# Kernel optimization log

Hardware: AMD Instinct MI355X
Metric: run time of the kernel (lower is better)

The kernel has to match this reference:

```python
import jax, jax.numpy as jnp
import numpy as np

B, S, D_MODEL, NUM_HEADS, MAX_LEN = 4, 1024, 1024, 16, 1024
D_HEAD = D_MODEL // NUM_HEADS


def _skew(QEr):
    # QEr: (b, h, s, s). Music-Transformer skew: pad one col on the left,
    # reshape swapping the last two dims, drop the first row.
    b, h, r, c = QEr.shape
    padded = jnp.pad(QEr, ((0, 0), (0, 0), (0, 0), (1, 0)))  # (b,h,r,c+1)
    reshaped = padded.reshape(b, h, c + 1, r)
    return reshaped[:, :, 1:, :]  # (b,h,s,s)


def setup_inputs() -> dict:
    key = jax.random.key(0)
    ks = jax.random.split(key, 8)
    sc = 1.0 / np.sqrt(D_MODEL).astype(np.float32)
    return {
        "x": jax.random.normal(ks[0], (B, S, D_MODEL), jnp.float32),
        "Wq": jax.random.normal(ks[1], (D_MODEL, D_MODEL), jnp.float32) * sc,
        "bq": jnp.zeros((D_MODEL,), jnp.float32),
        "Wk": jax.random.normal(ks[2], (D_MODEL, D_MODEL), jnp.float32) * sc,
        "bk": jnp.zeros((D_MODEL,), jnp.float32),
        "Wv": jax.random.normal(ks[3], (D_MODEL, D_MODEL), jnp.float32) * sc,
        "bv": jnp.zeros((D_MODEL,), jnp.float32),
        "Er": jax.random.normal(ks[4], (MAX_LEN, D_HEAD), jnp.float32),
    }


def reference(x, Wq, bq, Wk, bk, Wv, bv, Er):
    b, s, _ = x.shape
    h, dh = NUM_HEADS, D_HEAD
    # projections -> (b, h, s, dh). Weights stored [in, out] (equiv. to torch W.T).
    q = (x @ Wq + bq).reshape(b, s, h, dh).transpose(0, 2, 1, 3)
    k = (x @ Wk + bk).reshape(b, s, h, dh).transpose(0, 2, 1, 3)
    v = (x @ Wv + bv).reshape(b, s, h, dh).transpose(0, 2, 1, 3)
    Er_t = Er[MAX_LEN - s:, :]                      # (s, dh)
    QEr = jnp.einsum('bhsd,td->bhst', q, Er_t)      # (b,h,s,s)
    Srel = _skew(QEr)
    scores = (jnp.einsum('bhsd,bhtd->bhst', q, k) + Srel) / np.float32(np.sqrt(dh))
    causal = jnp.tril(jnp.ones((s, s), bool))       # (s,s)
    scores = jnp.where(causal[None, None], scores, -jnp.inf)
    attn = jax.nn.softmax(scores, axis=-1)
    out = jnp.einsum('bhst,bhtd->bhsd', attn, v)    # (b,h,s,dh)
    return out.transpose(0, 2, 1, 3).reshape(b, s, h * dh)
```

## Files before the change

kernel.cpp:

```cpp
#include <hip/hip_runtime.h>
#include <hip/hip_bf16.h>
#include <math.h>

typedef __attribute__((ext_vector_type(8))) short short8;
typedef __attribute__((ext_vector_type(4))) float f32x4;
typedef __attribute__((ext_vector_type(4))) unsigned short us4;

#define DM 1024
#define NH 16
#define DH 64
#define BB 4
#define SS 1024
#define SCALE 0.125f

#define GLDS16(g, l) __builtin_amdgcn_global_load_lds(                      \
    (const __attribute__((address_space(1))) unsigned int*)(g),             \
    (__attribute__((address_space(3))) unsigned int*)(l), 16, 0, 0)

__device__ __forceinline__ unsigned short f2b(float f){
    unsigned int u = __float_as_uint(f);
    u += 0x7fffu + ((u >> 16) & 1u);
    return (unsigned short)(u >> 16);
}
__device__ __forceinline__ float b2f(unsigned short b){
    return __uint_as_float(((unsigned int)b) << 16);
}

__global__ __launch_bounds__(256) void cast_f32_bf16_k(const float* __restrict__ in,
                                                       unsigned short* __restrict__ out){
    int i = (blockIdx.x * 256 + threadIdx.x) * 4;
    float4 v = *(const float4*)(in + i);
    us4 o = { f2b(v.x), f2b(v.y), f2b(v.z), f2b(v.w) };
    *(us4*)(out + i) = o;
}

__global__ __launch_bounds__(256) void transpose_cast_w_k(const float* __restrict__ Wq,
                                                          const float* __restrict__ Wk,
                                                          const float* __restrict__ Wv,
                                                          unsigned short* __restrict__ wT){
    __shared__ float tile[32][33];
    const float* W = blockIdx.z==0 ? Wq : (blockIdx.z==1 ? Wk : Wv);
    int o0 = blockIdx.x*32, k0 = blockIdx.y*32;
    int tx = threadIdx.x, ty = threadIdx.y;
    #pragma unroll
    for (int i=0;i<32;i+=8) tile[ty+i][tx] = W[(k0+ty+i)*DM + o0+tx];
    __syncthreads();
    #pragma unroll
    for (int i=0;i<32;i+=8) wT[(blockIdx.z*DM + o0+ty+i)*DM + k0+tx] = f2b(tile[tx][ty+i]);
}

__global__ __launch_bounds__(256) void gemm_qkv_k(
    const unsigned short* __restrict__ xb, const unsigned short* __restrict__ wT,
    const float* __restrict__ bq, const float* __restrict__ bk, const float* __restrict__ bv,
    unsigned short* __restrict__ Qb, unsigned short* __restrict__ Kb, unsigned short* __restrict__ Vb)
{
    __shared__ unsigned short lda[128*32];
    __shared__ unsigned short ldb[128*32];
    const int tid = threadIdx.x;
    const int lane = tid & 63, w = tid >> 6;
    const int wr = w >> 1, wc = w & 1;
    const int lr = lane & 15, lk = (lane >> 4) * 8;
    const int m0 = blockIdx.y * 128, n0 = blockIdx.x * 128;
    f32x4 acc[4][4] = {};
    for (int k0 = 0; k0 < DM; k0 += 32){
        #pragma unroll
        for (int p=0;p<2;p++){
            int idx = tid + p*256;
            int row = idx >> 2, cc = (idx & 3) * 8;
            GLDS16(&xb[(m0+row)*DM + k0 + cc], &lda[idx<<3]);
            GLDS16(&wT[(n0+row)*DM + k0 + cc], &ldb[idx<<3]);
        }
        __syncthreads();
        short8 a[4], b[4];
        #pragma unroll
        for (int m=0;m<4;m++) a[m] = *(const short8*)(&lda[(wr*64+m*16+lr)*32 + lk]);
        #pragma unroll
        for (int n=0;n<4;n++) b[n] = *(const short8*)(&ldb[(wc*64+n*16+lr)*32 + lk]);
        __builtin_amdgcn_s_setprio(1);
        #pragma unroll
        for (int m=0;m<4;m++)
            #pragma unroll
            for (int n=0;n<4;n++)
                acc[m][n] = __builtin_amdgcn_mfma_f32_16x16x32_bf16(a[m], b[n], acc[m][n], 0,0,0);
        __builtin_amdgcn_s_setprio(0);
        __syncthreads();
    }
    #pragma unroll
    for (int m=0;m<4;m++){
        #pragma unroll
        for (int n=0;n<4;n++){
            int C = n0 + wc*64 + n*16 + lr;
            int proj = C >> 10, hd = C & 1023;
            const float* bias = proj==0 ? bq : (proj==1 ? bk : bv);
            unsigned short* dst = proj==0 ? Qb : (proj==1 ? Kb : Vb);
            float badd = bias[hd];
            int h = hd >> 6, d = hd & 63;
            #pragma unroll
            for (int r=0;r<4;r++){
                int R = m0 + wr*64 + m*16 + (lane>>4)*4 + r;
                int b_ = R >> 10, s = R & 1023;
                dst[(((b_*NH)+h)*SS + s)*DH + d] = f2b(acc[m][n][r] + badd);
            }
        }
    }
}

__global__ __launch_bounds__(256) void attn_k(
    const unsigned short* __restrict__ Qb, const unsigned short* __restrict__ Kb,
    const unsigned short* __restrict__ Vb, const unsigned short* __restrict__ Erb,
    float* __restrict__ out)
{
    __shared__ unsigned short k_lds[64*64];
    __shared__ unsigned short vt_lds[64*64];
    __shared__ unsigned short er_lds[128*64];
    __shared__ unsigned short p_lds[64*64];
    __shared__ unsigned short rb_lds[4][16*80];

    const int tid = threadIdx.x, lane = tid & 63, w = tid >> 6;
    const int lr = lane & 15, lk4 = lane >> 4;
    const int bh = blockIdx.x;
    const int i0 = (int)(gridDim.y - 1 - blockIdx.y) * 64;
    const unsigned short* q_b = Qb + bh*SS*DH;
    const unsigned short* k_b = Kb + bh*SS*DH;
    const unsigned short* v_b = Vb + bh*SS*DH;

    short8 qf[2];
    #pragma unroll
    for (int kk=0;kk<2;kk++)
        qf[kk] = *(const short8*)(&q_b[(i0 + w*16 + lr)*DH + kk*32 + lk4*8]);

    const int vd = tid & 63, vjg = tid >> 6;

    f32x4 o_acc[4] = {};
    float m_r[4] = {-INFINITY,-INFINITY,-INFINITY,-INFINITY};
    float l_r[4] = {0.f,0.f,0.f,0.f};
    unsigned short* rbw = &rb_lds[w][0];
    const int fbase = 3 - w;

    const int ntiles = i0/64 + 1;
    for (int t=0; t<ntiles; t++){
        const int j0 = t*64;
        const int t0 = 960 - i0 + j0;
        __syncthreads();
        #pragma unroll
        for (int p=0;p<2;p++){
            int idx = tid + p*256;
            int row = idx >> 3, ch = idx & 7;
            GLDS16(&k_b[(j0+row)*DH + ((ch ^ (row&7))<<3)], &k_lds[idx<<3]);
        }
        #pragma unroll
        for (int p=0;p<4;p++){
            int idx = tid + p*256;
            int row = idx >> 3, ch = idx & 7;
            GLDS16(&Erb[(t0+row)*DH + ((ch ^ (row&7))<<3)], &er_lds[idx<<3]);
        }
        {
            unsigned short vv[16];
            #pragma unroll
            for (int jj=0;jj<16;jj++) vv[jj] = v_b[(j0 + vjg*16 + jj)*DH + vd];
            #pragma unroll
            for (int hh=0;hh<2;hh++){
                short8 pk;
                #pragma unroll
                for (int e=0;e<8;e++) pk[e] = (short)vv[hh*8+e];
                *(short8*)(&vt_lds[vd*64 + (((vjg*2+hh) ^ (vd&7))<<3)]) = pk;
            }
        }
        __syncthreads();

        f32x4 s_acc[4] = {};
        f32x4 r_acc[5] = {};
        __builtin_amdgcn_s_setprio(1);
        #pragma unroll
        for (int kk=0;kk<2;kk++){
            const int sco = ((kk*4+lk4) ^ (lr&7)) << 3;
            #pragma unroll
            for (int n=0;n<4;n++){
                short8 kf = *(const short8*)(&k_lds[(n*16+lr)*64 + sco]);
                s_acc[n] = __builtin_amdgcn_mfma_f32_16x16x32_bf16(qf[kk], kf, s_acc[n], 0,0,0);
            }
            #pragma unroll
            for (int fi=0;fi<5;fi++){
                short8 ef = *(const short8*)(&er_lds[((fbase+fi)*16+lr)*64 + sco]);
                r_acc[fi] = __builtin_amdgcn_mfma_f32_16x16x32_bf16(qf[kk], ef, r_acc[fi], 0,0,0);
            }
        }
        __builtin_amdgcn_s_setprio(0);

        #pragma unroll
        for (int fi=0;fi<5;fi++)
            #pragma unroll
            for (int r=0;r<4;r++)
                rbw[(lk4*4+r)*80 + fi*16 + lr] = f2b(r_acc[fi][r]);

        const bool lastt = (t == ntiles-1);
        #pragma unroll
        for (int r=0;r<4;r++){
            const int rr = lk4*4 + r;
            const int li = w*16 + rr;
            const int gi = i0 + li;
            float sv[4];
            float mx = -INFINITY;
            #pragma unroll
            for (int n=0;n<4;n++){
                float s = (s_acc[n][r] + b2f(rbw[rr*80 + 15 - rr + n*16 + lr])) * SCALE;
                if (lastt && (j0 + n*16 + lr > gi)) s = -INFINITY;
                sv[n] = s;
                mx = fmaxf(mx, s);
            }
            #pragma unroll
            for (int msk=1; msk<16; msk<<=1) mx = fmaxf(mx, __shfl_xor(mx, msk));
            float mnew = fmaxf(m_r[r], mx);
            float sfac = __expf(m_r[r] - mnew);
            m_r[r] = mnew;
            float rs = 0.f;
            #pragma unroll
            for (int n=0;n<4;n++){
                float p = __expf(sv[n] - mnew);
                rs += p;
                const int prow = li;
                p_lds[prow*64 + (((n*2 + (lr>>3)) ^ (prow&7))<<3) + (lr&7)] = f2b(p);
            }
            #pragma unroll
            for (int msk=1; msk<16; msk<<=1) rs += __shfl_xor(rs, msk);
            l_r[r] = l_r[r]*sfac + rs;
            #pragma unroll
            for (int n=0;n<4;n++) o_acc[n][r] *= sfac;
        }

        __builtin_amdgcn_s_setprio(1);
        #pragma unroll
        for (int kk=0;kk<2;kk++){
            const int sco = ((kk*4+lk4) ^ (lr&7)) << 3;
            short8 pf = *(const short8*)(&p_lds[(w*16+lr)*64 + sco]);
            #pragma unroll
            for (int n=0;n<4;n++){
                short8 vf = *(const short8*)(&vt_lds[(n*16+lr)*64 + sco]);
                o_acc[n] = __builtin_amdgcn_mfma_f32_16x16x32_bf16(pf, vf, o_acc[n], 0,0,0);
            }
        }
        __builtin_amdgcn_s_setprio(0);
    }
    const int b_ = bh >> 4, h = bh & 15;
    #pragma unroll
    for (int n=0;n<4;n++)
        #pragma unroll
        for (int r=0;r<4;r++){
            int li = w*16 + lk4*4 + r;
            int d = n*16 + lr;
            out[(b_*SS + i0 + li)*DM + h*DH + d] = o_acc[n][r] / l_r[r];
        }
}

extern "C" void kernel_launch(void* const* d_in, const int* in_sizes, int n_in,
                              void* d_out, int out_size, void* d_ws, size_t ws_size,
                              hipStream_t stream)
{
    const float* x  = (const float*)d_in[0];
    const float* Wq = (const float*)d_in[1];
    const float* bq = (const float*)d_in[2];
    const float* Wk = (const float*)d_in[3];
    const float* bk = (const float*)d_in[4];
    const float* Wv = (const float*)d_in[5];
    const float* bv = (const float*)d_in[6];
    const float* Er = (const float*)d_in[7];
    float* out = (float*)d_out;
    char* ws = (char*)d_ws;
    unsigned short* xb  = (unsigned short*)(ws);
    unsigned short* wT  = (unsigned short*)(ws + 8388608);
    unsigned short* erb = (unsigned short*)(ws + 14680064);
    unsigned short* Qb  = (unsigned short*)(ws + 14827520);
    unsigned short* Kb  = (unsigned short*)(ws + 23216128);
    unsigned short* Vb  = (unsigned short*)(ws + 31604736);

    cast_f32_bf16_k<<<4096, 256, 0, stream>>>(x, xb);
    cast_f32_bf16_k<<<64, 256, 0, stream>>>(Er, erb);
    hipMemsetAsync(erb + 1024*DH, 0, 128*DH*sizeof(unsigned short), stream);
    transpose_cast_w_k<<<dim3(32,32,3), dim3(32,8), 0, stream>>>(Wq, Wk, Wv, wT);
    gemm_qkv_k<<<dim3(24,32), 256, 0, stream>>>(xb, wT, bq, bk, bv, Qb, Kb, Vb);
    attn_k<<<dim3(64,16), 256, 0, stream>>>(Qb, Kb, Vb, erb, out);
}
```

Baseline: 103.5 us.

## Double-buffer K/V tiles, write V transposed from GEMM, use exp2 softmax

The QKV GEMM now writes V already transposed (d-major), so the attention kernel can stage V^T with async global-to-LDS loads instead of a per-thread gather and repack. K and V^T tiles are double-buffered and the next tile is prefetched while the current one is computed. Er staging is issued after a mid-loop barrier. Softmax now works in base 2 with the scale folded into the constant C2 and exp2, and the relative-bias scratch uses a transposed layout with packed 4-element stores. The transposed V store in the GEMM is strided and uncoalesced, and the extra LDS for double buffering may lower occupancy.

```diff
diff --git a/kernel.cpp b/kernel.cpp
--- a/kernel.cpp
+++ b/kernel.cpp
@@ -9,9 +9,8 @@
 #define DM 1024
 #define NH 16
 #define DH 64
-#define BB 4
 #define SS 1024
-#define SCALE 0.125f
+#define C2 0.180336879f
 
 #define GLDS16(g, l) __builtin_amdgcn_global_load_lds(                      \
     (const __attribute__((address_space(1))) unsigned int*)(g),             \
@@ -52,7 +51,7 @@
 __global__ __launch_bounds__(256) void gemm_qkv_k(
     const unsigned short* __restrict__ xb, const unsigned short* __restrict__ wT,
     const float* __restrict__ bq, const float* __restrict__ bk, const float* __restrict__ bv,
-    unsigned short* __restrict__ Qb, unsigned short* __restrict__ Kb, unsigned short* __restrict__ Vb)
+    unsigned short* __restrict__ Qb, unsigned short* __restrict__ Kb, unsigned short* __restrict__ VTb)
 {
     __shared__ unsigned short lda[128*32];
     __shared__ unsigned short ldb[128*32];
@@ -92,14 +91,16 @@
             int C = n0 + wc*64 + n*16 + lr;
             int proj = C >> 10, hd = C & 1023;
             const float* bias = proj==0 ? bq : (proj==1 ? bk : bv);
-            unsigned short* dst = proj==0 ? Qb : (proj==1 ? Kb : Vb);
             float badd = bias[hd];
             int h = hd >> 6, d = hd & 63;
             #pragma unroll
             for (int r=0;r<4;r++){
                 int R = m0 + wr*64 + m*16 + (lane>>4)*4 + r;
                 int b_ = R >> 10, s = R & 1023;
-                dst[(((b_*NH)+h)*SS + s)*DH + d] = f2b(acc[m][n][r] + badd);
+                unsigned short val = f2b(acc[m][n][r] + badd);
+                if (proj == 0)      Qb[(((b_*NH)+h)*SS + s)*DH + d] = val;
+                else if (proj == 1) Kb[(((b_*NH)+h)*SS + s)*DH + d] = val;
+                else                VTb[(((b_*NH)+h)*DH + d)*SS + s] = val;
             }
         }
     }
@@ -107,66 +108,61 @@
 
 __global__ __launch_bounds__(256) void attn_k(
     const unsigned short* __restrict__ Qb, const unsigned short* __restrict__ Kb,
-    const unsigned short* __restrict__ Vb, const unsigned short* __restrict__ Erb,
+    const unsigned short* __restrict__ VTb, const unsigned short* __restrict__ Erb,
     float* __restrict__ out)
 {
-    __shared__ unsigned short k_lds[64*64];
-    __shared__ unsigned short vt_lds[64*64];
+    __shared__ unsigned short k_lds[2][64*64];
+    __shared__ unsigned short vt_lds[2][64*64];
     __shared__ unsigned short er_lds[128*64];
     __shared__ unsigned short p_lds[64*64];
-    __shared__ unsigned short rb_lds[4][16*80];
+    __shared__ unsigned short rbt[4][80*20];
 
     const int tid = threadIdx.x, lane = tid & 63, w = tid >> 6;
     const int lr = lane & 15, lk4 = lane >> 4;
     const int bh = blockIdx.x;
     const int i0 = (int)(gridDim.y - 1 - blockIdx.y) * 64;
-    const unsigned short* q_b = Qb + bh*SS*DH;
-    const unsigned short* k_b = Kb + bh*SS*DH;
-    const unsigned short* v_b = Vb + bh*SS*DH;
-
-    short8 qf[2];
-    #pragma unroll
-    for (int kk=0;kk<2;kk++)
-        qf[kk] = *(const short8*)(&q_b[(i0 + w*16 + lr)*DH + kk*32 + lk4*8]);
-
-    const int vd = tid & 63, vjg = tid >> 6;
-
-    f32x4 o_acc[4] = {};
-    float m_r[4] = {-INFINITY,-INFINITY,-INFINITY,-INFINITY};
-    float l_r[4] = {0.f,0.f,0.f,0.f};
-    unsigned short* rbw = &rb_lds[w][0];
-    const int fbase = 3 - w;
-
-    const int ntiles = i0/64 + 1;
-    for (int t=0; t<ntiles; t++){
-        const int j0 = t*64;
-        const int t0 = 960 - i0 + j0;
-        __syncthreads();
+    const unsigned short* q_b  = Qb  + bh*SS*DH;
+    const unsigned short* k_b  = Kb  + bh*SS*DH;
+    const unsigned short* vt_b = VTb + bh*DH*SS;
+
+    auto STAGE_KVT = [&](int buf, int j0){
         #pragma unroll
         for (int p=0;p<2;p++){
             int idx = tid + p*256;
             int row = idx >> 3, ch = idx & 7;
-            GLDS16(&k_b[(j0+row)*DH + ((ch ^ (row&7))<<3)], &k_lds[idx<<3]);
-        }
+            GLDS16(&k_b[(j0+row)*DH + ((ch ^ (row&7))<<3)],  &k_lds[buf][idx<<3]);
+            GLDS16(&vt_b[row*SS + j0 + ((ch ^ (row&7))<<3)], &vt_lds[buf][idx<<3]);
+        }
+    };
+    auto STAGE_ER = [&](int t0){
         #pragma unroll
         for (int p=0;p<4;p++){
             int idx = tid + p*256;
             int row = idx >> 3, ch = idx & 7;
             GLDS16(&Erb[(t0+row)*DH + ((ch ^ (row&7))<<3)], &er_lds[idx<<3]);
         }
-        {
-            unsigned short vv[16];
-            #pragma unroll
-            for (int jj=0;jj<16;jj++) vv[jj] = v_b[(j0 + vjg*16 + jj)*DH + vd];
-            #pragma unroll
-            for (int hh=0;hh<2;hh++){
-                short8 pk;
-                #pragma unroll
-                for (int e=0;e<8;e++) pk[e] = (short)vv[hh*8+e];
-                *(short8*)(&vt_lds[vd*64 + (((vjg*2+hh) ^ (vd&7))<<3)]) = pk;
-            }
-        }
-        __syncthreads();
+    };
+
+    short8 qf[2];
+    #pragma unroll
+    for (int kk=0;kk<2;kk++)
+        qf[kk] = *(const short8*)(&q_b[(i0 + w*16 + lr)*DH + kk*32 + lk4*8]);
+
+    const int ntiles = i0/64 + 1;
+    STAGE_KVT(0, 0);
+    STAGE_ER(960 - i0);
+    __syncthreads();
+
+    f32x4 o_acc[4] = {};
+    float m2[4] = {-INFINITY,-INFINITY,-INFINITY,-INFINITY};
+    float l_r[4] = {0.f,0.f,0.f,0.f};
+    unsigned short* rbw = &rbt[w][0];
+    const int fbase = 3 - w;
+
+    for (int t=0; t<ntiles; t++){
+        const int cur = t & 1;
+        const int j0 = t*64;
+        if (t+1 < ntiles) STAGE_KVT(cur^1, j0+64);
 
         f32x4 s_acc[4] = {};
         f32x4 r_acc[5] = {};
@@ -176,7 +172,7 @@
             const int sco = ((kk*4+lk4) ^ (lr&7)) << 3;
             #pragma unroll
             for (int n=0;n<4;n++){
-                short8 kf = *(const short8*)(&k_lds[(n*16+lr)*64 + sco]);
+                short8 kf = *(const short8*)(&k_lds[cur][(n*16+lr)*64 + sco]);
                 s_acc[n] = __builtin_amdgcn_mfma_f32_16x16x32_bf16(qf[kk], kf, s_acc[n], 0,0,0);
             }
             #pragma unroll
@@ -187,11 +183,17 @@
         }
         __builtin_amdgcn_s_setprio(0);
 
-        #pragma unroll
-        for (int fi=0;fi<5;fi++)
-            #pragma unroll
-            for (int r=0;r<4;r++)
-                rbw[(lk4*4+r)*80 + fi*16 + lr] = f2b(r_acc[fi][r]);
+        asm volatile("" ::: "memory");
+        __builtin_amdgcn_s_barrier();
+        asm volatile("" ::: "memory");
+        if (t+1 < ntiles) STAGE_ER(960 - i0 + j0 + 64);
+
+        #pragma unroll
+        for (int fi=0;fi<5;fi++){
+            us4 pk = { f2b(r_acc[fi][0]*C2), f2b(r_acc[fi][1]*C2),
+                       f2b(r_acc[fi][2]*C2), f2b(r_acc[fi][3]*C2) };
+            *(us4*)(&rbw[(fi*16+lr)*20 + lk4*4]) = pk;
+        }
 
         const bool lastt = (t == ntiles-1);
         #pragma unroll
@@ -199,27 +201,26 @@
             const int rr = lk4*4 + r;
             const int li = w*16 + rr;
             const int gi = i0 + li;
-            float sv[4];
+            float s2[4];
             float mx = -INFINITY;
             #pragma unroll
             for (int n=0;n<4;n++){
-                float s = (s_acc[n][r] + b2f(rbw[rr*80 + 15 - rr + n*16 + lr])) * SCALE;
-                if (lastt && (j0 + n*16 + lr > gi)) s = -INFINITY;
-                sv[n] = s;
-                mx = fmaxf(mx, s);
+                float v = fmaf(s_acc[n][r], C2, b2f(rbw[(15 - rr + n*16 + lr)*20 + rr]));
+                if (lastt && (j0 + n*16 + lr > gi)) v = -INFINITY;
+                s2[n] = v;
+                mx = fmaxf(mx, v);
             }
             #pragma unroll
             for (int msk=1; msk<16; msk<<=1) mx = fmaxf(mx, __shfl_xor(mx, msk));
-            float mnew = fmaxf(m_r[r], mx);
-            float sfac = __expf(m_r[r] - mnew);
-            m_r[r] = mnew;
+            float mnew = fmaxf(m2[r], mx);
+            float sfac = __builtin_amdgcn_exp2f(m2[r] - mnew);
+            m2[r] = mnew;
             float rs = 0.f;
             #pragma unroll
             for (int n=0;n<4;n++){
-                float p = __expf(sv[n] - mnew);
+                float p = __builtin_amdgcn_exp2f(s2[n] - mnew);
                 rs += p;
-                const int prow = li;
-                p_lds[prow*64 + (((n*2 + (lr>>3)) ^ (prow&7))<<3) + (lr&7)] = f2b(p);
+                p_lds[li*64 + (((n*2 + (lr>>3)) ^ (li&7))<<3) + (lr&7)] = f2b(p);
             }
             #pragma unroll
             for (int msk=1; msk<16; msk<<=1) rs += __shfl_xor(rs, msk);
@@ -235,12 +236,14 @@
             short8 pf = *(const short8*)(&p_lds[(w*16+lr)*64 + sco]);
             #pragma unroll
             for (int n=0;n<4;n++){
-                short8 vf = *(const short8*)(&vt_lds[(n*16+lr)*64 + sco]);
+                short8 vf = *(const short8*)(&vt_lds[cur][(n*16+lr)*64 + sco]);
                 o_acc[n] = __builtin_amdgcn_mfma_f32_16x16x32_bf16(pf, vf, o_acc[n], 0,0,0);
             }
         }
         __builtin_amdgcn_s_setprio(0);
+        __syncthreads();
     }
+
     const int b_ = bh >> 4, h = bh & 15;
     #pragma unroll
     for (int n=0;n<4;n++)
@@ -271,12 +274,12 @@
     unsigned short* erb = (unsigned short*)(ws + 14680064);
     unsigned short* Qb  = (unsigned short*)(ws + 14827520);
     unsigned short* Kb  = (unsigned short*)(ws + 23216128);
-    unsigned short* Vb  = (unsigned short*)(ws + 31604736);
+    unsigned short* VTb = (unsigned short*)(ws + 31604736);
 
     cast_f32_bf16_k<<<4096, 256, 0, stream>>>(x, xb);
     cast_f32_bf16_k<<<64, 256, 0, stream>>>(Er, erb);
     hipMemsetAsync(erb + 1024*DH, 0, 128*DH*sizeof(unsigned short), stream);
     transpose_cast_w_k<<<dim3(32,32,3), dim3(32,8), 0, stream>>>(Wq, Wk, Wv, wT);
-    gemm_qkv_k<<<dim3(24,32), 256, 0, stream>>>(xb, wT, bq, bk, bv, Qb, Kb, Vb);
-    attn_k<<<dim3(64,16), 256, 0, stream>>>(Qb, Kb, Vb, erb, out);
-}
+    gemm_qkv_k<<<dim3(24,32), 256, 0, stream>>>(xb, wT, bq, bk, bv, Qb, Kb, VTb);
+    attn_k<<<dim3(64,16), 256, 0, stream>>>(Qb, Kb, VTb, erb, out);
+}
```

Result: slower. 112.1 us (+8.3%).
